# Performance work log

Hardware: AMD Instinct MI355X
Metric: run time of the kernel (lower is better)

Reference implementation:

```python
import jax, jax.numpy as jnp
import numpy as np

B = 16384
QD = 2048   # query_dim
KD = 1024   # key_dim
HID = 1024  # hidden_dim = min(QD, KD)
NH = 16     # num_heads
HD = HID // NH  # head_dim = 64
LN_EPS = 1e-5


def _ln(x, w, b):
    m = jnp.mean(x, axis=-1, keepdims=True)
    v = jnp.mean((x - m) ** 2, axis=-1, keepdims=True)
    return (x - m) * jax.lax.rsqrt(v + LN_EPS) * w + b


def _lin(x, W, b):
    return x @ W.T + b


def setup_inputs() -> dict:
    key = jax.random.key(0)
    ks = jax.random.split(key, 12)
    p = lambda k, shape: jax.random.normal(k, shape, jnp.float32) * 0.02
    return dict(
        query_features=jax.random.normal(ks[0], (B, QD), jnp.float32),
        key_features=jax.random.normal(ks[1], (B, KD), jnp.float32),
        Wq=p(ks[2], (HID, QD)), bq=jnp.zeros((HID,), jnp.float32),
        ln_q_w=jnp.ones((HID,), jnp.float32), ln_q_b=jnp.zeros((HID,), jnp.float32),
        Wk=p(ks[3], (HID, KD)), bk=jnp.zeros((HID,), jnp.float32),
        ln_k_w=jnp.ones((HID,), jnp.float32), ln_k_b=jnp.zeros((HID,), jnp.float32),
        Wvq=p(ks[4], (HID, QD)), bvq=jnp.zeros((HID,), jnp.float32),
        Wvk=p(ks[5], (HID, KD)), bvk=jnp.zeros((HID,), jnp.float32),
        Wo=p(ks[6], (QD, HID)), bo=jnp.zeros((QD,), jnp.float32),
        ln_o_w=jnp.ones((QD,), jnp.float32), ln_o_b=jnp.zeros((QD,), jnp.float32),
        Wg1=p(ks[7], (HID, QD + KD)), bg1=jnp.zeros((HID,), jnp.float32),
        Wg2=p(ks[8], (1, HID)), bg2=jnp.zeros((1,), jnp.float32),
        Wc1=p(ks[9], (HID, QD + KD)), bc1=jnp.zeros((HID,), jnp.float32),
        Wc2=p(ks[10], (1, HID)), bc2=jnp.zeros((1,), jnp.float32),
    )


def reference(query_features, key_features,
              Wq, bq, ln_q_w, ln_q_b,
              Wk, bk, ln_k_w, ln_k_b,
              Wvq, bvq, Wvk, bvk,
              Wo, bo, ln_o_w, ln_o_b,
              Wg1, bg1, Wg2, bg2,
              Wc1, bc1, Wc2, bc2):
    b = query_features.shape[0]
    q = _ln(_lin(query_features, Wq, bq), ln_q_w, ln_q_b)      # [B, HID]
    k = _ln(_lin(key_features, Wk, bk), ln_k_w, ln_k_b)        # [B, HID]
    v_q = _lin(query_features, Wvq, bvq)  # computed in torch but unused
    v_k = _lin(key_features, Wvk, bvk)    # [B, HID]
    q = q.reshape(b, NH, HD)
    k = k.reshape(b, NH, HD)
    v_k = v_k.reshape(b, NH, HD)
    # NOTE: attention mixes over the HEAD axis (j == num_heads), per original einsum
    scores = jnp.einsum('bhd,bjd->bhj', q, k) / np.sqrt(HD).astype(np.float32)
    attn = jax.nn.softmax(scores, axis=-1)  # dropout p effectively 0 / eval mode
    attended = jnp.einsum('bhj,bjd->bhd', attn, v_k).reshape(b, HID)
    output = _ln(_lin(attended, Wo, bo), ln_o_w, ln_o_b)       # [B, QD]
    combined = jnp.concatenate([query_features, key_features], axis=1)  # [B, QD+KD]
    gate = jax.nn.sigmoid(_lin(jax.nn.gelu(_lin(combined, Wg1, bg1), approximate=False), Wg2, bg2))
    chem = jax.nn.sigmoid(_lin(jax.nn.gelu(_lin(combined, Wc1, bc1), approximate=False), Wc2, bc2))
    effective_gate = gate * chem  # [B, 1]
    return query_features + effective_gate * output
```

## Files before the change

kernel.cpp:

```cpp
#include <hip/hip_runtime.h>
#include <stdint.h>

#define QD 2048
#define KD 1024
#define HID 1024
#define NH 16
#define HD 64
#define CMBD 3072

typedef float  f32x4   __attribute__((ext_vector_type(4)));
typedef short  short8  __attribute__((ext_vector_type(8)));
typedef short  short4v __attribute__((ext_vector_type(4)));
typedef float  float4v __attribute__((ext_vector_type(4)));

__device__ inline float bf2f(short s) {
  unsigned u = ((unsigned)(unsigned short)s) << 16;
  return __builtin_bit_cast(float, u);
}
__device__ inline short f2bf(float f) {
  unsigned u = __builtin_bit_cast(unsigned, f);
  u = u + 0x7fff + ((u >> 16) & 1);
  return (short)(u >> 16);
}

__global__ void cvt_bf16(const float* __restrict__ s, short* __restrict__ d) {
  size_t i = ((size_t)blockIdx.x * blockDim.x + threadIdx.x) * 4;
  float4v v = *(const float4v*)(s + i);
  short4v o;
  o[0] = f2bf(v[0]); o[1] = f2bf(v[1]); o[2] = f2bf(v[2]); o[3] = f2bf(v[3]);
  *(short4v*)(d + i) = o;
}

__global__ void cvt_concat(const float* __restrict__ s, short* __restrict__ d,
                           int ncols4, int ldd) {
  int i = blockIdx.x * blockDim.x + threadIdx.x;
  int row = i / ncols4;
  int c4  = i - row * ncols4;
  float4v v = *(const float4v*)(s + (size_t)row * (ncols4 * 4) + c4 * 4);
  short4v o;
  o[0] = f2bf(v[0]); o[1] = f2bf(v[1]); o[2] = f2bf(v[2]); o[3] = f2bf(v[3]);
  *(short4v*)(d + (size_t)row * ldd + c4 * 4) = o;
}

#define EPI_NONE 0
#define EPI_GELU 1

typedef const __attribute__((address_space(1))) void gvoid_t;
typedef __attribute__((address_space(3))) void lvoid_t;

#define WAIT_VM(n) asm volatile("s_waitcnt vmcnt(" #n ")" ::: "memory")

__device__ __forceinline__ void stage_half(short* sl, const short* A, size_t lda,
                                           const short* W, size_t ldw,
                                           size_t rowA, size_t rowB, int kbase, int tid) {
  const int grow  = tid >> 2;
  const int slotx = (tid & 3) ^ ((tid >> 3) & 3);
  const int gcol  = kbase + slotx * 8;
#pragma unroll
  for (int p = 0; p < 2; p++) {
    const short* ga = A + (rowA + p * 128 + grow) * lda + gcol;
    __builtin_amdgcn_global_load_lds((gvoid_t*)ga,
        (lvoid_t*)(sl + p * 4096 + tid * 8), 16, 0, 0);
    const short* gb = W + (rowB + p * 128 + grow) * ldw + gcol;
    __builtin_amdgcn_global_load_lds((gvoid_t*)gb,
        (lvoid_t*)(sl + 8192 + p * 4096 + tid * 8), 16, 0, 0);
  }
}

template<int EPI>
__global__ __launch_bounds__(512, 2)
void gemm256(const short* __restrict__ A, size_t lda,
             const short* __restrict__ W,
             const float* __restrict__ bias,
             short* __restrict__ C, int N, int K) {
  extern __shared__ short ls[];
  const int tid  = threadIdx.x;
  const int lane = tid & 63;
  const int wave = tid >> 6;
  const int wm = wave >> 2, wn = wave & 3;
  const int fr = lane & 15, kq4 = lane >> 4;

  const int nwg = gridDim.x * gridDim.y;
  const int lin = blockIdx.y * gridDim.x + blockIdx.x;
  const int cpx = nwg >> 3;
  const int nid = (lin & 7) * cpx + (lin >> 3);
  const int bx = nid % gridDim.x, by = nid / gridDim.x;
  const size_t rowBase = (size_t)by * 256;
  const size_t colBase = (size_t)bx * 256;

  const int NK2 = K >> 5;

  f32x4 acc[8][4];
#pragma unroll
  for (int mi = 0; mi < 8; mi++)
#pragma unroll
    for (int ni = 0; ni < 4; ni++) acc[mi][ni] = (f32x4){0.f, 0.f, 0.f, 0.f};

  const int slot_x = (fr >> 1) & 3;
  const int axk = (kq4 ^ slot_x) * 8;
  const int abase = (wm * 128 + fr) * 32 + axk;
  const int bbase = (wn * 64 + fr) * 32 + axk;

  stage_half(ls + 0 * 16384, A, lda, W, (size_t)K, rowBase, colBase, 0, tid);
  stage_half(ls + 1 * 16384, A, lda, W, (size_t)K, rowBase, colBase, 32, tid);
  stage_half(ls + 2 * 16384, A, lda, W, (size_t)K, rowBase, colBase, 64, tid);
  WAIT_VM(8);
  __builtin_amdgcn_s_barrier();

  for (int h = 0; h < NK2; ++h) {
    const short* sl = ls + (h & 3) * 16384;
    short8 af[8], bf[4];
#pragma unroll
    for (int mi = 0; mi < 8; mi++)
      af[mi] = *(const short8*)(sl + abase + mi * 512);
#pragma unroll
    for (int ni = 0; ni < 4; ni++)
      bf[ni] = *(const short8*)(sl + 8192 + bbase + ni * 512);

    if (h + 3 < NK2)
      stage_half(ls + ((h + 3) & 3) * 16384, A, lda, W, (size_t)K,
                 rowBase, colBase, (h + 3) * 32, tid);

    __builtin_amdgcn_s_setprio(1);
#pragma unroll
    for (int mi = 0; mi < 8; mi++)
#pragma unroll
      for (int ni = 0; ni < 4; ni++)
        acc[mi][ni] = __builtin_amdgcn_mfma_f32_16x16x32_bf16(af[mi], bf[ni], acc[mi][ni], 0, 0, 0);
    __builtin_amdgcn_s_setprio(0);

    asm volatile("s_waitcnt lgkmcnt(0)" ::: "memory");
    const int rem = NK2 - 2 - h;
    if (rem >= 2)      { WAIT_VM(8); }
    else if (rem == 1) { WAIT_VM(4); }
    else               { WAIT_VM(0); }
    __builtin_amdgcn_s_barrier();
  }

#pragma unroll
  for (int mi = 0; mi < 8; mi++) {
    const size_t row0 = rowBase + wm * 128 + mi * 16 + kq4 * 4;
#pragma unroll
    for (int ni = 0; ni < 4; ni++) {
      const int col = (int)colBase + wn * 64 + ni * 16 + fr;
      const float bv = bias[col];
#pragma unroll
      for (int j = 0; j < 4; j++) {
        float x = acc[mi][ni][j] + bv;
        if (EPI == EPI_GELU) x = 0.5f * x * (1.f + erff(x * 0.70710678118f));
        C[(row0 + j) * (size_t)N + col] = f2bf(x);
      }
    }
  }
}

__device__ inline float2 block_sum2(float a, float b, float* sc) {
#pragma unroll
  for (int o = 32; o >= 1; o >>= 1) {
    a += __shfl_down(a, o);
    b += __shfl_down(b, o);
  }
  const int lane = threadIdx.x & 63, w = threadIdx.x >> 6;
  const int nw = blockDim.x >> 6;
  if (lane == 0) { sc[w * 2] = a; sc[w * 2 + 1] = b; }
  __syncthreads();
  float ra = 0.f, rb = 0.f;
  for (int i = 0; i < nw; i++) { ra += sc[i * 2]; rb += sc[i * 2 + 1]; }
  __syncthreads();
  return make_float2(ra, rb);
}

__global__ __launch_bounds__(256)
void attn_ln(const short* __restrict__ qp, const short* __restrict__ kv,
             const float* __restrict__ lnqw, const float* __restrict__ lnqb,
             const float* __restrict__ lnkw, const float* __restrict__ lnkb,
             short* __restrict__ att) {
  __shared__ float qs[HID];
  __shared__ float ks[NH * 65];
  __shared__ float vs[HID];
  __shared__ float aw[256];
  __shared__ float red[8];
  const int t = threadIdx.x;
  const size_t row = blockIdx.x;

  short4v q4 = *(const short4v*)(qp + row * HID + t * 4);
  short4v k4 = *(const short4v*)(kv + row * 2048 + t * 4);
  short4v v4 = *(const short4v*)(kv + row * 2048 + 1024 + t * 4);
  float qv[4], kvv[4];
  float sq = 0.f, sqq = 0.f, sk = 0.f, skk = 0.f;
#pragma unroll
  for (int i = 0; i < 4; i++) {
    qv[i] = bf2f(q4[i]); sq += qv[i]; sqq += qv[i] * qv[i];
    kvv[i] = bf2f(k4[i]); sk += kvv[i]; skk += kvv[i] * kvv[i];
  }
  float2 rq = block_sum2(sq, sqq, red);
  float mq = rq.x / HID, vq = rq.y / HID - mq * mq;
  float rsq = rsqrtf(vq + 1e-5f);
  float2 rk = block_sum2(sk, skk, red);
  float mk = rk.x / HID, vv = rk.y / HID - mk * mk;
  float rsk = rsqrtf(vv + 1e-5f);
#pragma unroll
  for (int i = 0; i < 4; i++) {
    const int idx = t * 4 + i;
    qs[idx] = (qv[i] - mq) * rsq * lnqw[idx] + lnqb[idx];
    ks[(idx >> 6) * 65 + (idx & 63)] = (kvv[i] - mk) * rsk * lnkw[idx] + lnkb[idx];
    vs[idx] = bf2f(v4[i]);
  }
  __syncthreads();

  const int h = t >> 4, j = t & 15;
  float s = 0.f;
#pragma unroll 8
  for (int d = 0; d < 64; d++) s += qs[h * 64 + d] * ks[j * 65 + d];
  s *= 0.125f;
  float mx = s;
#pragma unroll
  for (int o = 8; o >= 1; o >>= 1) mx = fmaxf(mx, __shfl_xor(mx, o, 16));
  float e = __expf(s - mx);
  float sum = e;
#pragma unroll
  for (int o = 8; o >= 1; o >>= 1) sum += __shfl_xor(sum, o, 16);
  aw[t] = e / sum;
  __syncthreads();

  const int dB = (t & 15) * 4;
  float o0 = 0.f, o1 = 0.f, o2 = 0.f, o3 = 0.f;
#pragma unroll
  for (int jj = 0; jj < 16; jj++) {
    const float w = aw[h * 16 + jj];
    const float* vp = &vs[jj * 64 + dB];
    o0 += w * vp[0]; o1 += w * vp[1]; o2 += w * vp[2]; o3 += w * vp[3];
  }
  short4v o4;
  o4[0] = f2bf(o0); o4[1] = f2bf(o1); o4[2] = f2bf(o2); o4[3] = f2bf(o3);
  *(short4v*)(att + row * HID + h * 64 + dB) = o4;
}

__global__ __launch_bounds__(256)
void gate_kernel(const short* __restrict__ hgc,
                 const float* __restrict__ wg2, const float* __restrict__ bg2,
                 const float* __restrict__ wc2, const float* __restrict__ bc2,
                 float* __restrict__ eg) {
  __shared__ float red[8];
  const int t = threadIdx.x;
  const size_t row = blockIdx.x;
  short4v g4 = *(const short4v*)(hgc + row * 2048 + t * 4);
  short4v c4 = *(const short4v*)(hgc + row * 2048 + 1024 + t * 4);
  float sg = 0.f, sc = 0.f;
#pragma unroll
  for (int i = 0; i < 4; i++) {
    sg += bf2f(g4[i]) * wg2[t * 4 + i];
    sc += bf2f(c4[i]) * wc2[t * 4 + i];
  }
  float2 r = block_sum2(sg, sc, red);
  if (t == 0) {
    float g = 1.f / (1.f + __expf(-(r.x + bg2[0])));
    float c = 1.f / (1.f + __expf(-(r.y + bc2[0])));
    eg[row] = g * c;
  }
}

__global__ __launch_bounds__(256)
void final_kernel(const short* __restrict__ opre, const float* __restrict__ qf,
                  const float* __restrict__ eg,
                  const float* __restrict__ lnow, const float* __restrict__ lnob,
                  float* __restrict__ out) {
  __shared__ float red[8];
  const int t = threadIdx.x;
  const size_t row = blockIdx.x;
  short8 o8 = *(const short8*)(opre + row * QD + t * 8);
  float x[8];
  float s = 0.f, ss = 0.f;
#pragma unroll
  for (int i = 0; i < 8; i++) { x[i] = bf2f(o8[i]); s += x[i]; ss += x[i] * x[i]; }
  float2 r = block_sum2(s, ss, red);
  float m = r.x / QD, v = r.y / QD - m * m;
  float rs = rsqrtf(v + 1e-5f);
  float g = eg[row];
  float4v oa, ob;
#pragma unroll
  for (int i = 0; i < 8; i++) {
    const int c = t * 8 + i;
    float y = (x[i] - m) * rs * lnow[c] + lnob[c];
    float r2 = qf[row * QD + c] + g * y;
    if (i < 4) oa[i] = r2; else ob[i - 4] = r2;
  }
  *(float4v*)(out + row * QD + t * 8) = oa;
  *(float4v*)(out + row * QD + t * 8 + 4) = ob;
}

extern "C" void kernel_launch(void* const* d_in, const int* in_sizes, int n_in,
                              void* d_out, int out_size, void* d_ws, size_t ws_size,
                              hipStream_t stream) {
  const float* qf   = (const float*)d_in[0];
  const float* kf   = (const float*)d_in[1];
  const float* Wq   = (const float*)d_in[2];
  const float* bq   = (const float*)d_in[3];
  const float* lnqw = (const float*)d_in[4];
  const float* lnqb = (const float*)d_in[5];
  const float* Wk   = (const float*)d_in[6];
  const float* bk   = (const float*)d_in[7];
  const float* lnkw = (const float*)d_in[8];
  const float* lnkb = (const float*)d_in[9];
  const float* Wvk  = (const float*)d_in[12];
  const float* bvk  = (const float*)d_in[13];
  const float* Wo   = (const float*)d_in[14];
  const float* bo   = (const float*)d_in[15];
  const float* lnow = (const float*)d_in[16];
  const float* lnob = (const float*)d_in[17];
  const float* Wg1  = (const float*)d_in[18];
  const float* bg1  = (const float*)d_in[19];
  const float* Wg2  = (const float*)d_in[20];
  const float* bg2  = (const float*)d_in[21];
  const float* Wc1  = (const float*)d_in[22];
  const float* bc1  = (const float*)d_in[23];
  const float* Wc2  = (const float*)d_in[24];
  const float* bc2  = (const float*)d_in[25];

  const int rows = in_sizes[0] / QD;

  char* ws = (char*)d_ws;
  size_t off = 0;
  auto alloc = [&](size_t bytes) -> char* {
    char* p = ws + off;
    off += (bytes + 255) & ~(size_t)255;
    return p;
  };
  short* cmb  = (short*)alloc((size_t)rows * CMBD * 2);
  short* wqb  = (short*)alloc((size_t)HID * QD * 2);
  short* wkv  = (short*)alloc((size_t)2 * HID * KD * 2);
  short* wob  = (short*)alloc((size_t)QD * HID * 2);
  short* wgc  = (short*)alloc((size_t)2 * HID * CMBD * 2);
  short* hgc  = (short*)alloc((size_t)rows * 2048 * 2);
  short* qp   = (short*)alloc((size_t)rows * HID * 2);
  short* kvp  = (short*)alloc((size_t)rows * 2048 * 2);
  float* eg   = (float*)alloc((size_t)rows * 4);
  float* bgc  = (float*)alloc(2048 * 4);
  float* bkv  = (float*)alloc(2048 * 4);
  short* att  = hgc;
  short* opre = cmb;

  hipMemcpyAsync(bgc, bg1, HID * 4, hipMemcpyDeviceToDevice, stream);
  hipMemcpyAsync(bgc + HID, bc1, HID * 4, hipMemcpyDeviceToDevice, stream);
  hipMemcpyAsync(bkv, bk, HID * 4, hipMemcpyDeviceToDevice, stream);
  hipMemcpyAsync(bkv + HID, bvk, HID * 4, hipMemcpyDeviceToDevice, stream);

  cvt_concat<<<rows * 2, 256, 0, stream>>>(qf, cmb, QD / 4, CMBD);
  cvt_concat<<<rows, 256, 0, stream>>>(kf, cmb + QD, KD / 4, CMBD);
  cvt_bf16<<<(HID * QD / 4) / 256, 256, 0, stream>>>(Wq, wqb);
  cvt_bf16<<<(HID * KD / 4) / 256, 256, 0, stream>>>(Wk, wkv);
  cvt_bf16<<<(HID * KD / 4) / 256, 256, 0, stream>>>(Wvk, wkv + (size_t)HID * KD);
  cvt_bf16<<<(QD * HID / 4) / 256, 256, 0, stream>>>(Wo, wob);
  cvt_bf16<<<(HID * CMBD / 4) / 256, 256, 0, stream>>>(Wg1, wgc);
  cvt_bf16<<<(HID * CMBD / 4) / 256, 256, 0, stream>>>(Wc1, wgc + (size_t)HID * CMBD);

  hipFuncSetAttribute((const void*)gemm256<EPI_GELU>,
                      hipFuncAttributeMaxDynamicSharedMemorySize, 131072);
  hipFuncSetAttribute((const void*)gemm256<EPI_NONE>,
                      hipFuncAttributeMaxDynamicSharedMemorySize, 131072);

  const dim3 blk(512);
  const int mt = rows / 256;
  const size_t lds = 131072;

  gemm256<EPI_GELU><<<dim3(2048 / 256, mt), blk, lds, stream>>>(cmb, CMBD, wgc, bgc, hgc, 2048, CMBD);
  gate_kernel<<<rows, 256, 0, stream>>>(hgc, Wg2, bg2, Wc2, bc2, eg);
  gemm256<EPI_NONE><<<dim3(1024 / 256, mt), blk, lds, stream>>>(cmb, CMBD, wqb, bq, qp, 1024, QD);
  gemm256<EPI_NONE><<<dim3(2048 / 256, mt), blk, lds, stream>>>(cmb + QD, CMBD, wkv, bkv, kvp, 2048, KD);
  attn_ln<<<rows, 256, 0, stream>>>(qp, kvp, lnqw, lnqb, lnkw, lnkb, att);
  gemm256<EPI_NONE><<<dim3(2048 / 256, mt), blk, lds, stream>>>(att, HID, wob, bo, opre, 2048, HID);
  final_kernel<<<rows, 256, 0, stream>>>(opre, qf, eg, lnow, lnob, (float*)d_out);
}
```

Measured before the change: 657.1 us.

## Restructure GEMM main loop into split A/B staging with triple buffering

The bf16 GEMM moves from a 4-stage LDS ring with prefetch depth 3 to a 3-stage ring with prefetch depth 2. Each k-step is split into two halves: the A tile is staged while the first 4 row-fragments are multiplied, and the W tile is staged while the second 4 are multiplied, with barriers and sched_barriers between the halves. This cuts LDS per block from 128 KB to 96 KB and lowers register pressure because fewer A fragments are live at once, which could help occupancy. In exchange there are more barriers per iteration and less latency hiding from the shallower prefetch.

Result: no change. 662.4 us (+0.8%).

```diff
diff --git a/kernel.cpp b/kernel.cpp
--- a/kernel.cpp
+++ b/kernel.cpp
@@ -48,22 +48,19 @@
 typedef const __attribute__((address_space(1))) void gvoid_t;
 typedef __attribute__((address_space(3))) void lvoid_t;
 
-#define WAIT_VM(n) asm volatile("s_waitcnt vmcnt(" #n ")" ::: "memory")
-
-__device__ __forceinline__ void stage_half(short* sl, const short* A, size_t lda,
-                                           const short* W, size_t ldw,
-                                           size_t rowA, size_t rowB, int kbase, int tid) {
+#define WAIT_VM(n)  asm volatile("s_waitcnt vmcnt(" #n ")" ::: "memory")
+#define WAIT_LGKM0  asm volatile("s_waitcnt lgkmcnt(0)" ::: "memory")
+
+__device__ __forceinline__ void stage_op(short* dst, const short* G, size_t ldg,
+                                         size_t rowBase, int kt, int tid) {
   const int grow  = tid >> 2;
   const int slotx = (tid & 3) ^ ((tid >> 3) & 3);
-  const int gcol  = kbase + slotx * 8;
-#pragma unroll
-  for (int p = 0; p < 2; p++) {
-    const short* ga = A + (rowA + p * 128 + grow) * lda + gcol;
-    __builtin_amdgcn_global_load_lds((gvoid_t*)ga,
-        (lvoid_t*)(sl + p * 4096 + tid * 8), 16, 0, 0);
-    const short* gb = W + (rowB + p * 128 + grow) * ldw + gcol;
-    __builtin_amdgcn_global_load_lds((gvoid_t*)gb,
-        (lvoid_t*)(sl + 8192 + p * 4096 + tid * 8), 16, 0, 0);
+  const int gcol  = kt + slotx * 8;
+#pragma unroll
+  for (int l = 0; l < 2; l++) {
+    const short* g = G + (rowBase + l * 128 + grow) * ldg + gcol;
+    __builtin_amdgcn_global_load_lds((gvoid_t*)g,
+        (lvoid_t*)(dst + l * 4096 + tid * 8), 16, 0, 0);
   }
 }
 
@@ -88,7 +85,7 @@
   const size_t rowBase = (size_t)by * 256;
   const size_t colBase = (size_t)bx * 256;
 
-  const int NK2 = K >> 5;
+  const int NT = K >> 5;
 
   f32x4 acc[8][4];
 #pragma unroll
@@ -96,45 +93,59 @@
 #pragma unroll
     for (int ni = 0; ni < 4; ni++) acc[mi][ni] = (f32x4){0.f, 0.f, 0.f, 0.f};
 
-  const int slot_x = (fr >> 1) & 3;
-  const int axk = (kq4 ^ slot_x) * 8;
-  const int abase = (wm * 128 + fr) * 32 + axk;
-  const int bbase = (wn * 64 + fr) * 32 + axk;
-
-  stage_half(ls + 0 * 16384, A, lda, W, (size_t)K, rowBase, colBase, 0, tid);
-  stage_half(ls + 1 * 16384, A, lda, W, (size_t)K, rowBase, colBase, 32, tid);
-  stage_half(ls + 2 * 16384, A, lda, W, (size_t)K, rowBase, colBase, 64, tid);
-  WAIT_VM(8);
+  const int frsw = (kq4 ^ ((fr >> 1) & 3)) * 8;
+  const int aoff = (wm * 128 + fr) * 32 + frsw;
+  const int boff = 8192 + (wn * 64 + fr) * 32 + frsw;
+
+  stage_op(ls + 0 * 16384,        A, lda,       rowBase, 0,  tid);
+  stage_op(ls + 0 * 16384 + 8192, W, (size_t)K, colBase, 0,  tid);
+  stage_op(ls + 1 * 16384,        A, lda,       rowBase, 32, tid);
+  stage_op(ls + 1 * 16384 + 8192, W, (size_t)K, colBase, 32, tid);
+  WAIT_VM(4);
   __builtin_amdgcn_s_barrier();
 
-  for (int h = 0; h < NK2; ++h) {
-    const short* sl = ls + (h & 3) * 16384;
-    short8 af[8], bf[4];
-#pragma unroll
-    for (int mi = 0; mi < 8; mi++)
-      af[mi] = *(const short8*)(sl + abase + mi * 512);
-#pragma unroll
-    for (int ni = 0; ni < 4; ni++)
-      bf[ni] = *(const short8*)(sl + 8192 + bbase + ni * 512);
-
-    if (h + 3 < NK2)
-      stage_half(ls + ((h + 3) & 3) * 16384, A, lda, W, (size_t)K,
-                 rowBase, colBase, (h + 3) * 32, tid);
-
+  int rb = 0, sb = 2;
+  for (int t = 0; t < NT; ++t) {
+    const short* sl = ls + rb * 16384;
+    short* st = ls + sb * 16384;
+    const bool dostage = (t + 2 < NT);
+    short8 af[4], bf[4];
+
+#pragma unroll
+    for (int m = 0; m < 4; m++) af[m] = *(const short8*)(sl + aoff + m * 512);
+#pragma unroll
+    for (int n = 0; n < 4; n++) bf[n] = *(const short8*)(sl + boff + n * 512);
+    if (dostage) stage_op(st, A, lda, rowBase, (t + 2) * 32, tid);
+    __builtin_amdgcn_s_barrier();
+    WAIT_LGKM0;
+    __builtin_amdgcn_sched_barrier(0);
     __builtin_amdgcn_s_setprio(1);
 #pragma unroll
-    for (int mi = 0; mi < 8; mi++)
-#pragma unroll
-      for (int ni = 0; ni < 4; ni++)
-        acc[mi][ni] = __builtin_amdgcn_mfma_f32_16x16x32_bf16(af[mi], bf[ni], acc[mi][ni], 0, 0, 0);
+    for (int m = 0; m < 4; m++)
+#pragma unroll
+      for (int n = 0; n < 4; n++)
+        acc[m][n] = __builtin_amdgcn_mfma_f32_16x16x32_bf16(af[m], bf[n], acc[m][n], 0, 0, 0);
     __builtin_amdgcn_s_setprio(0);
-
-    asm volatile("s_waitcnt lgkmcnt(0)" ::: "memory");
-    const int rem = NK2 - 2 - h;
-    if (rem >= 2)      { WAIT_VM(8); }
-    else if (rem == 1) { WAIT_VM(4); }
-    else               { WAIT_VM(0); }
     __builtin_amdgcn_s_barrier();
+
+#pragma unroll
+    for (int m = 0; m < 4; m++) af[m] = *(const short8*)(sl + aoff + (m + 4) * 512);
+    if (dostage) stage_op(st + 8192, W, (size_t)K, colBase, (t + 2) * 32, tid);
+    __builtin_amdgcn_s_barrier();
+    WAIT_LGKM0;
+    __builtin_amdgcn_sched_barrier(0);
+    __builtin_amdgcn_s_setprio(1);
+#pragma unroll
+    for (int m = 0; m < 4; m++)
+#pragma unroll
+      for (int n = 0; n < 4; n++)
+        acc[m + 4][n] = __builtin_amdgcn_mfma_f32_16x16x32_bf16(af[m], bf[n], acc[m + 4][n], 0, 0, 0);
+    __builtin_amdgcn_s_setprio(0);
+    if (dostage) { WAIT_VM(4); } else { WAIT_VM(0); }
+    __builtin_amdgcn_s_barrier();
+
+    rb = (rb == 2) ? 0 : rb + 1;
+    sb = (sb == 2) ? 0 : sb + 1;
   }
 
 #pragma unroll
@@ -355,13 +366,13 @@
   cvt_bf16<<<(HID * CMBD / 4) / 256, 256, 0, stream>>>(Wc1, wgc + (size_t)HID * CMBD);
 
   hipFuncSetAttribute((const void*)gemm256<EPI_GELU>,
-                      hipFuncAttributeMaxDynamicSharedMemorySize, 131072);
+                      hipFuncAttributeMaxDynamicSharedMemorySize, 98304);
   hipFuncSetAttribute((const void*)gemm256<EPI_NONE>,
-                      hipFuncAttributeMaxDynamicSharedMemorySize, 131072);
+                      hipFuncAttributeMaxDynamicSharedMemorySize, 98304);
 
   const dim3 blk(512);
   const int mt = rows / 256;
-  const size_t lds = 131072;
+  const size_t lds = 98304;
 
   gemm256<EPI_GELU><<<dim3(2048 / 256, mt), blk, lds, stream>>>(cmb, CMBD, wgc, bgc, hgc, 2048, CMBD);
   gate_kernel<<<rows, 256, 0, stream>>>(hgc, Wg2, bg2, Wc2, bc2, eg);
```
